# Performance work log

Measured on AMD Instinct MI355X. Metric: run time of the kernel, lower is better.

The kernel has to match this reference:

```python
import jax, jax.numpy as jnp
import numpy as np


def setup_inputs() -> dict:
    key = jax.random.key(0)
    k1, k2 = jax.random.split(key)
    B, N, M, D = 4, 8192, 8192, 3
    ground_truth = jax.random.normal(k1, (B, N, D), dtype=jnp.float32)
    reconstruction = jax.random.normal(k2, (B, M, D), dtype=jnp.float32)
    return {"ground_truth": ground_truth, "reconstruction": reconstruction}


def reference(ground_truth, reconstruction):
    x, y = ground_truth, reconstruction  # [B,N,D], [B,M,D]
    xx = jnp.sum(x * x, axis=-1)                      # [B,N]
    yy = jnp.sum(y * y, axis=-1)                      # [B,M]
    xy = jnp.einsum('bnd,bmd->bnm', x, y)             # [B,N,M]
    P = xx[:, :, None] + yy[:, None, :] - 2.0 * xy    # [B,N,M]
    # clamp(min=1e-10) then mean, in both directions
    loss_1 = jnp.mean(jnp.maximum(jnp.min(P, axis=1), 1e-10))
    loss_2 = jnp.mean(jnp.maximum(jnp.min(P, axis=2), 1e-10))
    total = (loss_1 + loss_2) * 1000.0
    return total
```

## Files before the change

### kernel.cpp

```cpp
#include <hip/hip_runtime.h>

typedef _Float16 half_t;
typedef _Float16 f16x4 __attribute__((ext_vector_type(4)));
typedef _Float16 f16x8 __attribute__((ext_vector_type(8)));
typedef float f32x16 __attribute__((ext_vector_type(16)));

#define BATCH 4
#define NPTS 8192
#define NSEG 128
#define MSEG 2048
#define CHUNK_M 1024
#define NTILES 32
#define NCHUNKS (MSEG / CHUNK_M)

#if __has_builtin(__builtin_amdgcn_mfma_f32_32x32x8f16)
static __device__ __forceinline__ f32x16 MFMA8(f16x4 a, f16x4 b, f32x16 c) {
    return __builtin_amdgcn_mfma_f32_32x32x8f16(a, b, c, 0, 0, 0);
}
#else
static __device__ __forceinline__ f32x16 MFMA8(f16x4 a, f16x4 b, f32x16 c) {
    f16x8 a8 = {a[0], a[1], a[2], a[3], (half_t)0.f, (half_t)0.f, (half_t)0.f, (half_t)0.f};
    f16x8 b8 = {b[0], b[1], b[2], b[3], (half_t)0.f, (half_t)0.f, (half_t)0.f, (half_t)0.f};
    return __builtin_amdgcn_mfma_f32_32x32x16_f16(a8, b8, c, 0, 0, 0);
}
#endif

static __device__ __forceinline__ float tree16(const f32x16& d) {
    float t0 = fminf(fminf(d[0], d[1]), d[2]);
    float t1 = fminf(fminf(d[3], d[4]), d[5]);
    float t2 = fminf(fminf(d[6], d[7]), d[8]);
    float t3 = fminf(fminf(d[9], d[10]), d[11]);
    float t4 = fminf(fminf(d[12], d[13]), d[14]);
    float u0 = fminf(fminf(t0, t1), t2);
    float u1 = fminf(fminf(t3, t4), d[15]);
    return fminf(u0, u1);
}

__global__ __launch_bounds__(256, 4) void chamfer_mfma_kernel(
    const float* __restrict__ gt, const float* __restrict__ rec,
    unsigned int* __restrict__ minbuf)
{
    const int nseg = blockIdx.x;
    const int mseg = blockIdx.y;
    const int b    = blockIdx.z;
    const float* G = gt  + (size_t)b * NPTS * 3;
    const float* R = rec + (size_t)b * NPTS * 3;
    const int n0 = nseg * NSEG;
    const int m0 = mseg * MSEG;

    const int tid  = threadIdx.x;
    const int lane = tid & 63;
    const int w    = tid >> 6;
    const int lr   = lane & 31;
    const int lh   = lane >> 5;

    __shared__ unsigned int rowbuf[MSEG];
    __shared__ float2 bfrag[NTILES][64];

    for (int i = tid; i < MSEG; i += 256) rowbuf[i] = 0x7F7F7F7Fu;

    f16x4 afrag;
    {
        int n = n0 + w * 32 + lr;
        float gx = G[n*3+0], gy = G[n*3+1], gz = G[n*3+2];
        half_t hx = (half_t)gx, hy = (half_t)gy, hz = (half_t)gz;
        float fx = (float)hx, fy = (float)hy, fz = (float)hz;
        float nrm = fx*fx + fy*fy + fz*fz;
        half_t nhi = (half_t)nrm;
        half_t nlo = (half_t)(nrm - (float)nhi);
        if (lh == 0) { afrag[0]=hx;  afrag[1]=hy;          afrag[2]=hz;          afrag[3]=nhi; }
        else         { afrag[0]=nlo; afrag[1]=(half_t)1.f; afrag[2]=(half_t)1.f; afrag[3]=(half_t)0.f; }
    }

    f32x16 colacc;
    #pragma unroll
    for (int i = 0; i < 16; ++i) colacc[i] = 3.0e38f;
    const f32x16 zc = {};

    float2 pref[6];
    auto loadpts = [&](int ch) {
        int m = m0 + ch * CHUNK_M + tid * 4;
        const float2* p = (const float2*)R + (size_t)(m * 3) / 2;
        #pragma unroll
        for (int k = 0; k < 6; ++k) pref[k] = p[k];
    };
    auto writepack = [&]() {
        float px[4], py[4], pz[4];
        px[0]=pref[0].x; py[0]=pref[0].y; pz[0]=pref[1].x;
        px[1]=pref[1].y; py[1]=pref[2].x; pz[1]=pref[2].y;
        px[2]=pref[3].x; py[2]=pref[3].y; pz[2]=pref[4].x;
        px[3]=pref[4].y; py[3]=pref[5].x; pz[3]=pref[5].y;
        #pragma unroll
        for (int s = 0; s < 4; ++s) {
            int j = tid * 4 + s;
            half_t hx = (half_t)px[s], hy = (half_t)py[s], hz = (half_t)pz[s];
            float fx = (float)hx, fy = (float)hy, fz = (float)hz;
            float nrm = fx*fx + fy*fy + fz*fz;
            half_t mhi = (half_t)nrm;
            half_t mlo = (half_t)(nrm - (float)mhi);
            union { half_t h[4]; float2 f; } u0, u1;
            u0.h[0] = (half_t)(-2.f*fx); u0.h[1] = (half_t)(-2.f*fy);
            u0.h[2] = (half_t)(-2.f*fz); u0.h[3] = (half_t)1.f;
            u1.h[0] = (half_t)1.f; u1.h[1] = mhi; u1.h[2] = mlo; u1.h[3] = (half_t)0.f;
            int t = j >> 5, c = j & 31;
            bfrag[t][c]      = u0.f;
            bfrag[t][c + 32] = u1.f;
        }
    };

    auto process2 = [&](const f32x16& da, const f32x16& db, int mba, int mbb) {
        #pragma unroll
        for (int i = 0; i < 16; ++i)
            colacc[i] = fminf(fminf(colacc[i], da[i]), db[i]);
        atomicMin(&rowbuf[mba + lr], __float_as_uint(tree16(da)));
        atomicMin(&rowbuf[mbb + lr], __float_as_uint(tree16(db)));
    };

    union { float2 f; f16x4 h; } cv;

    loadpts(0);
    for (int ch = 0; ch < NCHUNKS; ++ch) {
        __syncthreads();
        writepack();
        __syncthreads();
        if (ch + 1 < NCHUNKS) loadpts(ch + 1);
        const int mbase = ch * CHUNK_M;

        cv.f = bfrag[0][lane]; f16x4 b0 = cv.h;
        cv.f = bfrag[1][lane]; f16x4 b1 = cv.h;
        f32x16 d0 = MFMA8(afrag, b0, zc);
        f32x16 d1 = MFMA8(afrag, b1, zc);
        #pragma unroll
        for (int t = 2; t < NTILES; t += 2) {
            cv.f = bfrag[t][lane];     f16x4 ba = cv.h;
            cv.f = bfrag[t + 1][lane]; f16x4 bb = cv.h;
            f32x16 na = MFMA8(afrag, ba, zc);
            f32x16 nb = MFMA8(afrag, bb, zc);
            process2(d0, d1, mbase + (t - 2) * 32, mbase + (t - 1) * 32);
            d0 = na; d1 = nb;
        }
        process2(d0, d1, mbase + (NTILES - 2) * 32, mbase + (NTILES - 1) * 32);
    }
    __syncthreads();

    unsigned int* mb0 = minbuf + (size_t)b * NPTS;
    for (int i = tid; i < MSEG; i += 256)
        atomicMin(&mb0[m0 + i], rowbuf[i]);

    #pragma unroll
    for (int i = 0; i < 16; ++i) {
        float v = colacc[i];
        v = fminf(v, __shfl_xor(v, 1));
        v = fminf(v, __shfl_xor(v, 2));
        v = fminf(v, __shfl_xor(v, 4));
        v = fminf(v, __shfl_xor(v, 8));
        v = fminf(v, __shfl_xor(v, 16));
        colacc[i] = v;
    }
    unsigned int* mb1 = minbuf + (size_t)(BATCH + b) * NPTS;
    if (lr == 0) {
        #pragma unroll
        for (int i = 0; i < 16; ++i) {
            int r = (i & 3) + 8 * (i >> 2) + 4 * lh;
            atomicMin(&mb1[n0 + w * 32 + r], __float_as_uint(colacc[i]));
        }
    }
}

__global__ __launch_bounds__(256) void chamfer_init_kernel(
    unsigned int* __restrict__ minbuf, float* __restrict__ out)
{
    int idx = (blockIdx.x * 256 + threadIdx.x) * 4;
    *(uint4*)&minbuf[idx] = make_uint4(0x7F7F7F7Fu, 0x7F7F7F7Fu, 0x7F7F7F7Fu, 0x7F7F7F7Fu);
    if (blockIdx.x == 0 && threadIdx.x == 0) out[0] = 0.0f;
}

__global__ __launch_bounds__(256) void chamfer_reduce_kernel(
    const unsigned int* __restrict__ minbuf, float* __restrict__ out)
{
    int idx = (blockIdx.x * 256 + threadIdx.x) * 4;
    uint4 v = *(const uint4*)&minbuf[idx];
    float s = fmaxf(__uint_as_float(v.x), 1e-10f)
            + fmaxf(__uint_as_float(v.y), 1e-10f)
            + fmaxf(__uint_as_float(v.z), 1e-10f)
            + fmaxf(__uint_as_float(v.w), 1e-10f);
    #pragma unroll
    for (int off = 32; off > 0; off >>= 1) s += __shfl_down(s, off);
    __shared__ float ws4[4];
    int wv = threadIdx.x >> 6, ln = threadIdx.x & 63;
    if (ln == 0) ws4[wv] = s;
    __syncthreads();
    if (threadIdx.x == 0) {
        float tot = ws4[0] + ws4[1] + ws4[2] + ws4[3];
        atomicAdd(out, tot * (1000.0f / 32768.0f));
    }
}

extern "C" void kernel_launch(void* const* d_in, const int* in_sizes, int n_in,
                              void* d_out, int out_size, void* d_ws, size_t ws_size,
                              hipStream_t stream) {
    const float* gt  = (const float*)d_in[0];
    const float* rec = (const float*)d_in[1];
    unsigned int* minbuf = (unsigned int*)d_ws;

    const int TOT = 2 * BATCH * NPTS;
    chamfer_init_kernel<<<TOT / (256 * 4), 256, 0, stream>>>(minbuf, (float*)d_out);

    dim3 grid(NPTS / NSEG, NPTS / MSEG, BATCH);
    chamfer_mfma_kernel<<<grid, 256, 0, stream>>>(gt, rec, minbuf);

    chamfer_reduce_kernel<<<TOT / (256 * 4), 256, 0, stream>>>(minbuf, (float*)d_out);
}
```

Baseline: 74.81 us.

## Compute each chamfer direction separately with register-only column mins and fused reduction

Instead of one pass that yields both row and column minima through LDS atomics and global atomicMin buffers, the kernel now runs two passes, one per direction. Each block owns a segment of query points, scans all candidate points, and keeps minima only in registers. The clamp-and-sum reduction is folded into the same kernel and the init/reduce kernels are replaced by a memset. This doubles the MFMA work but removes the shared-memory atomics, the tree reductions and the extra launches.

```diff
diff --git a/kernel.cpp b/kernel.cpp
--- a/kernel.cpp
+++ b/kernel.cpp
@@ -7,11 +7,10 @@
 
 #define BATCH 4
 #define NPTS 8192
-#define NSEG 128
-#define MSEG 2048
-#define CHUNK_M 1024
+#define QSEG 128
+#define CHUNK 1024
 #define NTILES 32
-#define NCHUNKS (MSEG / CHUNK_M)
+#define NCH (NPTS / CHUNK)
 
 #if __has_builtin(__builtin_amdgcn_mfma_f32_32x32x8f16)
 static __device__ __forceinline__ f32x16 MFMA8(f16x4 a, f16x4 b, f32x16 c) {
@@ -25,28 +24,17 @@
 }
 #endif
 
-static __device__ __forceinline__ float tree16(const f32x16& d) {
-    float t0 = fminf(fminf(d[0], d[1]), d[2]);
-    float t1 = fminf(fminf(d[3], d[4]), d[5]);
-    float t2 = fminf(fminf(d[6], d[7]), d[8]);
-    float t3 = fminf(fminf(d[9], d[10]), d[11]);
-    float t4 = fminf(fminf(d[12], d[13]), d[14]);
-    float u0 = fminf(fminf(t0, t1), t2);
-    float u1 = fminf(fminf(t3, t4), d[15]);
-    return fminf(u0, u1);
-}
-
-__global__ __launch_bounds__(256, 4) void chamfer_mfma_kernel(
+__global__ __launch_bounds__(256, 2) void chamfer_kernel(
     const float* __restrict__ gt, const float* __restrict__ rec,
-    unsigned int* __restrict__ minbuf)
+    float* __restrict__ out)
 {
-    const int nseg = blockIdx.x;
-    const int mseg = blockIdx.y;
-    const int b    = blockIdx.z;
-    const float* G = gt  + (size_t)b * NPTS * 3;
-    const float* R = rec + (size_t)b * NPTS * 3;
-    const int n0 = nseg * NSEG;
-    const int m0 = mseg * MSEG;
+    const int qseg = blockIdx.x;
+    const int b    = blockIdx.y;
+    const int dir  = blockIdx.z;
+    const float* Q = (dir == 0) ? rec : gt;
+    const float* C = (dir == 0) ? gt  : rec;
+    Q += (size_t)b * NPTS * 3;
+    C += (size_t)b * NPTS * 3;
 
     const int tid  = threadIdx.x;
     const int lane = tid & 63;
@@ -54,16 +42,14 @@
     const int lr   = lane & 31;
     const int lh   = lane >> 5;
 
-    __shared__ unsigned int rowbuf[MSEG];
     __shared__ float2 bfrag[NTILES][64];
-
-    for (int i = tid; i < MSEG; i += 256) rowbuf[i] = 0x7F7F7F7Fu;
+    __shared__ float  wsum[4];
 
     f16x4 afrag;
     {
-        int n = n0 + w * 32 + lr;
-        float gx = G[n*3+0], gy = G[n*3+1], gz = G[n*3+2];
-        half_t hx = (half_t)gx, hy = (half_t)gy, hz = (half_t)gz;
+        int q = qseg * QSEG + w * 32 + lr;
+        float qx = Q[q*3+0], qy = Q[q*3+1], qz = Q[q*3+2];
+        half_t hx = (half_t)qx, hy = (half_t)qy, hz = (half_t)qz;
         float fx = (float)hx, fy = (float)hy, fz = (float)hz;
         float nrm = fx*fx + fy*fy + fz*fz;
         half_t nhi = (half_t)nrm;
@@ -79,8 +65,8 @@
 
     float2 pref[6];
     auto loadpts = [&](int ch) {
-        int m = m0 + ch * CHUNK_M + tid * 4;
-        const float2* p = (const float2*)R + (size_t)(m * 3) / 2;
+        int m = ch * CHUNK + tid * 4;
+        const float2* p = (const float2*)C + (size_t)(m * 3) / 2;
         #pragma unroll
         for (int k = 0; k < 6; ++k) pref[k] = p[k];
     };
@@ -108,23 +94,14 @@
         }
     };
 
-    auto process2 = [&](const f32x16& da, const f32x16& db, int mba, int mbb) {
-        #pragma unroll
-        for (int i = 0; i < 16; ++i)
-            colacc[i] = fminf(fminf(colacc[i], da[i]), db[i]);
-        atomicMin(&rowbuf[mba + lr], __float_as_uint(tree16(da)));
-        atomicMin(&rowbuf[mbb + lr], __float_as_uint(tree16(db)));
-    };
-
     union { float2 f; f16x4 h; } cv;
 
     loadpts(0);
-    for (int ch = 0; ch < NCHUNKS; ++ch) {
+    for (int ch = 0; ch < NCH; ++ch) {
         __syncthreads();
         writepack();
         __syncthreads();
-        if (ch + 1 < NCHUNKS) loadpts(ch + 1);
-        const int mbase = ch * CHUNK_M;
+        if (ch + 1 < NCH) loadpts(ch + 1);
 
         cv.f = bfrag[0][lane]; f16x4 b0 = cv.h;
         cv.f = bfrag[1][lane]; f16x4 b1 = cv.h;
@@ -136,17 +113,17 @@
             cv.f = bfrag[t + 1][lane]; f16x4 bb = cv.h;
             f32x16 na = MFMA8(afrag, ba, zc);
             f32x16 nb = MFMA8(afrag, bb, zc);
-            process2(d0, d1, mbase + (t - 2) * 32, mbase + (t - 1) * 32);
+            #pragma unroll
+            for (int i = 0; i < 16; ++i)
+                colacc[i] = fminf(fminf(colacc[i], d0[i]), d1[i]);
             d0 = na; d1 = nb;
         }
-        process2(d0, d1, mbase + (NTILES - 2) * 32, mbase + (NTILES - 1) * 32);
+        #pragma unroll
+        for (int i = 0; i < 16; ++i)
+            colacc[i] = fminf(fminf(colacc[i], d0[i]), d1[i]);
     }
-    __syncthreads();
 
-    unsigned int* mb0 = minbuf + (size_t)b * NPTS;
-    for (int i = tid; i < MSEG; i += 256)
-        atomicMin(&mb0[m0 + i], rowbuf[i]);
-
+    float s = 0.0f;
     #pragma unroll
     for (int i = 0; i < 16; ++i) {
         float v = colacc[i];
@@ -155,43 +132,13 @@
         v = fminf(v, __shfl_xor(v, 4));
         v = fminf(v, __shfl_xor(v, 8));
         v = fminf(v, __shfl_xor(v, 16));
-        colacc[i] = v;
+        s += fmaxf(v, 1e-10f);
     }
-    unsigned int* mb1 = minbuf + (size_t)(BATCH + b) * NPTS;
-    if (lr == 0) {
-        #pragma unroll
-        for (int i = 0; i < 16; ++i) {
-            int r = (i & 3) + 8 * (i >> 2) + 4 * lh;
-            atomicMin(&mb1[n0 + w * 32 + r], __float_as_uint(colacc[i]));
-        }
-    }
-}
-
-__global__ __launch_bounds__(256) void chamfer_init_kernel(
-    unsigned int* __restrict__ minbuf, float* __restrict__ out)
-{
-    int idx = (blockIdx.x * 256 + threadIdx.x) * 4;
-    *(uint4*)&minbuf[idx] = make_uint4(0x7F7F7F7Fu, 0x7F7F7F7Fu, 0x7F7F7F7Fu, 0x7F7F7F7Fu);
-    if (blockIdx.x == 0 && threadIdx.x == 0) out[0] = 0.0f;
-}
-
-__global__ __launch_bounds__(256) void chamfer_reduce_kernel(
-    const unsigned int* __restrict__ minbuf, float* __restrict__ out)
-{
-    int idx = (blockIdx.x * 256 + threadIdx.x) * 4;
-    uint4 v = *(const uint4*)&minbuf[idx];
-    float s = fmaxf(__uint_as_float(v.x), 1e-10f)
-            + fmaxf(__uint_as_float(v.y), 1e-10f)
-            + fmaxf(__uint_as_float(v.z), 1e-10f)
-            + fmaxf(__uint_as_float(v.w), 1e-10f);
-    #pragma unroll
-    for (int off = 32; off > 0; off >>= 1) s += __shfl_down(s, off);
-    __shared__ float ws4[4];
-    int wv = threadIdx.x >> 6, ln = threadIdx.x & 63;
-    if (ln == 0) ws4[wv] = s;
+    s += __shfl_xor(s, 32);
+    if (lane == 0) wsum[w] = s;
     __syncthreads();
-    if (threadIdx.x == 0) {
-        float tot = ws4[0] + ws4[1] + ws4[2] + ws4[3];
+    if (tid == 0) {
+        float tot = wsum[0] + wsum[1] + wsum[2] + wsum[3];
         atomicAdd(out, tot * (1000.0f / 32768.0f));
     }
 }
@@ -201,13 +148,10 @@
                               hipStream_t stream) {
     const float* gt  = (const float*)d_in[0];
     const float* rec = (const float*)d_in[1];
-    unsigned int* minbuf = (unsigned int*)d_ws;
+    (void)d_ws; (void)ws_size;
 
-    const int TOT = 2 * BATCH * NPTS;
-    chamfer_init_kernel<<<TOT / (256 * 4), 256, 0, stream>>>(minbuf, (float*)d_out);
+    hipMemsetAsync(d_out, 0, sizeof(float), stream);
 
-    dim3 grid(NPTS / NSEG, NPTS / MSEG, BATCH);
-    chamfer_mfma_kernel<<<grid, 256, 0, stream>>>(gt, rec, minbuf);
-
-    chamfer_reduce_kernel<<<TOT / (256 * 4), 256, 0, stream>>>(minbuf, (float*)d_out);
+    dim3 grid(NPTS / QSEG, BATCH, 2);
+    chamfer_kernel<<<grid, 256, 0, stream>>>(gt, rec, (float*)d_out);
 }
```

After: 77.81 us. 4.0% more time.
